# Performance work log

Hardware: AMD Instinct MI355X
Metric: run time of the kernel (lower is better)

Reference implementation:

```python
import jax, jax.numpy as jnp
import numpy as np

N, E, IN_DIM, HID, HEADS = 50000, 800000, 128, 16, 8
EPS_BN = 1e-5


def _gat_conv(x, edge_index, W, att_src, att_dst, bias, heads, out_ch, concat):
    # x: [N, F_in]; W: [heads*out_ch, F_in]; att_*: [heads, out_ch]
    n = x.shape[0]
    h = (x @ W.T).reshape(n, heads, out_ch)            # [N, H, C]
    a_src = (h * att_src[None]).sum(-1)                # [N, H]
    a_dst = (h * att_dst[None]).sum(-1)                # [N, H]
    src, dst = edge_index[0], edge_index[1]
    alpha = jax.nn.leaky_relu(a_src[src] + a_dst[dst], negative_slope=0.2)  # [E, H]
    # segment softmax over destination node (per head)
    amax = jax.ops.segment_max(alpha, dst, num_segments=n)
    amax = jnp.where(jnp.isfinite(amax), amax, 0.0)
    ex = jnp.exp(alpha - amax[dst])
    denom = jax.ops.segment_sum(ex, dst, num_segments=n)
    attn = ex / (denom[dst] + 1e-16)                   # [E, H]
    msg = h[src] * attn[:, :, None]                    # [E, H, C]
    out = jax.ops.segment_sum(msg, dst, num_segments=n)  # [N, H, C]
    out = out.reshape(n, heads * out_ch) if concat else out.mean(axis=1)
    return out + bias


def _bn_eval(h, mean, var, gamma, beta):
    return (h - mean) * jax.lax.rsqrt(var + EPS_BN) * gamma + beta


def setup_inputs() -> dict:
    key = jax.random.key(0)
    ks = jax.random.split(key, 16)
    s = 0.1
    inp = {
        "x": jax.random.normal(ks[0], (N, IN_DIM), jnp.float32),
        "edge_index": jax.random.randint(ks[1], (2, E), 0, N, jnp.int32),
        # layer 0: GATConv(128 -> 16, heads=8, concat)
        "w0": jax.random.normal(ks[2], (HEADS * HID, IN_DIM), jnp.float32) * s,
        "asrc0": jax.random.normal(ks[3], (HEADS, HID), jnp.float32) * s,
        "adst0": jax.random.normal(ks[4], (HEADS, HID), jnp.float32) * s,
        "b0": jnp.zeros((HEADS * HID,), jnp.float32),
        "skip0": jax.random.normal(ks[5], (HEADS * HID, IN_DIM), jnp.float32) * s,
        "bn0_g": jnp.ones((HEADS * HID,), jnp.float32),
        "bn0_b": jnp.zeros((HEADS * HID,), jnp.float32),
        "bn0_m": jax.random.normal(ks[6], (HEADS * HID,), jnp.float32) * s,
        "bn0_v": jax.random.uniform(ks[7], (HEADS * HID,), jnp.float32, 0.5, 1.5),
        # layer 1: GATConv(128 -> 16, heads=1, concat=False)
        "w1": jax.random.normal(ks[8], (HID, HEADS * HID), jnp.float32) * s,
        "asrc1": jax.random.normal(ks[9], (1, HID), jnp.float32) * s,
        "adst1": jax.random.normal(ks[10], (1, HID), jnp.float32) * s,
        "b1": jnp.zeros((HID,), jnp.float32),
        "skip1": jax.random.normal(ks[11], (HID, HEADS * HID), jnp.float32) * s,
        "bn1_g": jnp.ones((HID,), jnp.float32),
        "bn1_b": jnp.zeros((HID,), jnp.float32),
        "bn1_m": jax.random.normal(ks[12], (HID,), jnp.float32) * s,
        "bn1_v": jax.random.uniform(ks[13], (HID,), jnp.float32, 0.5, 1.5),
    }
    return inp


def reference(x, edge_index, w0, asrc0, adst0, b0, skip0, bn0_g, bn0_b, bn0_m, bn0_v,
              w1, asrc1, adst1, b1, skip1, bn1_g, bn1_b, bn1_m, bn1_v):
    # eval mode: dropout = identity, BN uses running stats
    h_in = x
    h = _gat_conv(h_in, edge_index, w0, asrc0, adst0, b0, HEADS, HID, True)   # [N, 128]
    h = _bn_eval(h, bn0_m, bn0_v, bn0_g, bn0_b)
    h = h + h_in @ skip0.T
    h = jax.nn.elu(h)
    h_in = h
    h = _gat_conv(h_in, edge_index, w1, asrc1, adst1, b1, 1, HID, False)      # [N, 16]
    h = _bn_eval(h, bn1_m, bn1_v, bn1_g, bn1_b)
    h = h + h_in @ skip1.T
    h = jax.nn.elu(h)
    return h
```

## Files before the change

### kernel.cpp

```cpp
#include <hip/hip_runtime.h>
#include <hip/hip_bf16.h>

#define NN 50000
#define EE 800000
#define INDIM 128
#define HIDC 16
#define NHEAD 8
#define COARSE 196
#define EPB 2048
#define CAPR 6144
#define CAPB 8192
#define CVT_BLKS 37

typedef __attribute__((ext_vector_type(8))) short bf16x8;
typedef __attribute__((ext_vector_type(4))) float f32x4;

__device__ __forceinline__ float bf2f(unsigned short u) {
    union { float f; unsigned int i; } v; v.i = ((unsigned int)u) << 16; return v.f;
}
__device__ __forceinline__ unsigned short f2bf(float f) {
    union { float f; unsigned int i; } v; v.f = f;
    unsigned int r = v.i + 0x7FFFu + ((v.i >> 16) & 1u);
    return (unsigned short)(r >> 16);
}

__global__ __launch_bounds__(256) void k_prep(
    const float* __restrict__ w0, const float* __restrict__ skip0,
    const float* __restrict__ w1, const float* __restrict__ skip1,
    const float* __restrict__ b0, const float* __restrict__ g0,
    const float* __restrict__ bb0, const float* __restrict__ m0,
    const float* __restrict__ v0,
    const float* __restrict__ b1, const float* __restrict__ g1,
    const float* __restrict__ bb1, const float* __restrict__ m1,
    const float* __restrict__ v1,
    unsigned int* __restrict__ wb2, unsigned int* __restrict__ wb1_2,
    float2* __restrict__ acb0, float2* __restrict__ acb1,
    const int* __restrict__ ei, int* __restrict__ ccur0,
    unsigned int* __restrict__ pairs)
{
    if (blockIdx.x < CVT_BLKS) {
        const long NW = 256 * 128 / 4;
        const long NW1 = 32 * 128 / 4;
        long i = (long)blockIdx.x * 256 + threadIdx.x;
        if (i < NW) {
            const float4* src = (i < 128 * 128 / 4) ? ((const float4*)w0 + i)
                                                    : ((const float4*)skip0 + (i - 128 * 128 / 4));
            float4 v = *src;
            wb2[i * 2]     = (unsigned int)f2bf(v.x) | ((unsigned int)f2bf(v.y) << 16);
            wb2[i * 2 + 1] = (unsigned int)f2bf(v.z) | ((unsigned int)f2bf(v.w) << 16);
        } else if (i < NW + NW1) {
            long j = i - NW;
            const float4* src = (j < 16 * 128 / 4) ? ((const float4*)w1 + j)
                                                   : ((const float4*)skip1 + (j - 16 * 128 / 4));
            float4 v = *src;
            wb1_2[j * 2]     = (unsigned int)f2bf(v.x) | ((unsigned int)f2bf(v.y) << 16);
            wb1_2[j * 2 + 1] = (unsigned int)f2bf(v.z) | ((unsigned int)f2bf(v.w) << 16);
        } else if (i < NW + NW1 + 128) {
            int c = (int)(i - NW - NW1);
            float A = g0[c] * rsqrtf(v0[c] + 1e-5f);
            acb0[c] = make_float2(A, (b0[c] - m0[c]) * A + bb0[c]);
        } else if (i < NW + NW1 + 128 + 16) {
            int c = (int)(i - NW - NW1 - 128);
            float A = g1[c] * rsqrtf(v1[c] + 1e-5f);
            acb1[c] = make_float2(A, (b1[c] - m1[c]) * A + bb1[c]);
        }
        return;
    }

    __shared__ int bcnt[256];
    __shared__ int lofs[256];
    __shared__ int gofs[256];
    __shared__ unsigned int stage[EPB];
    __shared__ int gpos[EPB];
    const int t = threadIdx.x;
    const int e0 = (blockIdx.x - CVT_BLKS) * EPB;

    bcnt[t] = 0;
    __syncthreads();

    int mybin[8], myrank[8];
    unsigned int mypair[8];
    #pragma unroll
    for (int k = 0; k < 8; k++) {
        int e = e0 + k * 256 + t;
        mybin[k] = -1;
        if (e < EE) {
            int s = ei[e], d = ei[EE + e];
            int b = d >> 8;
            myrank[k] = atomicAdd(&bcnt[b], 1);
            mybin[k] = b;
            mypair[k] = ((unsigned)d << 16) | (unsigned)s;
        }
    }
    __syncthreads();

    int v = bcnt[t];
    lofs[t] = v;
    __syncthreads();
    for (int off = 1; off < 256; off <<= 1) {
        int u = (t >= off) ? lofs[t - off] : 0;
        __syncthreads();
        lofs[t] += u;
        __syncthreads();
    }
    if (t < COARSE && v > 0)
        gofs[t] = t * CAPR + atomicAdd(&ccur0[t], v);
    __syncthreads();

    #pragma unroll
    for (int k = 0; k < 8; k++) {
        int b = mybin[k];
        if (b >= 0) {
            int slot = (lofs[b] - bcnt[b]) + myrank[k];
            stage[slot] = mypair[k];
            gpos[slot]  = gofs[b] + myrank[k];
        }
    }
    __syncthreads();

    const int total = lofs[255];
    for (int i = t; i < total; i += 256)
        pairs[gpos[i]] = stage[i];
}

__global__ __launch_bounds__(256) void k_mid(
    const unsigned int* __restrict__ pairs, const int* __restrict__ ccur0,
    unsigned short* __restrict__ srcidx, int* __restrict__ rowbeg,
    int* __restrict__ deg,
    const float* __restrict__ x, const unsigned short* __restrict__ wb,
    const float* __restrict__ asrc0, const float* __restrict__ adst0,
    unsigned char* __restrict__ h0f, unsigned short* __restrict__ s0b,
    float* __restrict__ a_src0, float* __restrict__ a_dst0)
{
    __shared__ int fcnt[256], fofs[256], fcur[256];
    __shared__ unsigned short stage[CAPB];

    if (blockIdx.x < COARSE) {
        const int b = blockIdx.x, t = threadIdx.x;
        const int beg = b * CAPR;
        int cnt = ccur0[b];
        if (cnt > CAPR) cnt = CAPR;

        fcnt[t] = 0;
        __syncthreads();
        for (int i = t; i < cnt; i += 256) {
            unsigned int d = pairs[beg + i] >> 16;
            atomicAdd(&fcnt[d & 255], 1);
        }
        __syncthreads();

        int v = fcnt[t];
        fofs[t] = v;
        __syncthreads();
        for (int off = 1; off < 256; off <<= 1) {
            int u = (t >= off) ? fofs[t - off] : 0;
            __syncthreads();
            fofs[t] += u;
            __syncthreads();
        }
        int ex = fofs[t] - v;
        int node = b * 256 + t;
        if (node < NN) { rowbeg[node] = beg + ex; deg[node] = v; }
        fcur[t] = ex;
        __syncthreads();

        for (int i = t; i < cnt; i += 256) {
            unsigned int p = pairs[beg + i];
            unsigned int d = p >> 16;
            int slot = atomicAdd(&fcur[d & 255], 1);
            stage[slot] = (unsigned short)(p & 0xFFFFu);
        }
        __syncthreads();
        for (int i = t; i < cnt; i += 256)
            srcidx[beg + i] = stage[i];
        return;
    }

    const int bid = blockIdx.x - COARSE;
    const int wave = threadIdx.x >> 6;
    const int lane = threadIdx.x & 63;
    const int lrow = lane & 15;
    const int quad = lane >> 4;
    const int rowbase = bid * 32;

    bf16x8 afrag[2][4];
    #pragma unroll
    for (int sub = 0; sub < 2; sub++) {
        const int row = min(rowbase + sub * 16 + lrow, NN - 1);
        const float* xr = x + (long)row * 128;
        #pragma unroll
        for (int ki = 0; ki < 4; ki++) {
            float4 a = *(const float4*)(xr + ki * 32 + quad * 8);
            float4 b = *(const float4*)(xr + ki * 32 + quad * 8 + 4);
            bf16x8 f;
            f[0] = (short)f2bf(a.x); f[1] = (short)f2bf(a.y);
            f[2] = (short)f2bf(a.z); f[3] = (short)f2bf(a.w);
            f[4] = (short)f2bf(b.x); f[5] = (short)f2bf(b.y);
            f[6] = (short)f2bf(b.z); f[7] = (short)f2bf(b.w);
            afrag[sub][ki] = f;
        }
    }

    #pragma unroll
    for (int t = 0; t < 4; t++) {
        const int jg = wave * 64 + t * 16 + lrow;
        bf16x8 bfrag[4];
        #pragma unroll
        for (int ki = 0; ki < 4; ki++)
            bfrag[ki] = *(const bf16x8*)(wb + (long)jg * 128 + ki * 32 + quad * 8);
        float4 asv = {0.f, 0.f, 0.f, 0.f}, adv = {0.f, 0.f, 0.f, 0.f};
        if (wave < 2) {
            const int cb = wave * 64 + t * 16 + quad * 4;
            asv = *(const float4*)(asrc0 + cb);
            adv = *(const float4*)(adst0 + cb);
        }
        #pragma unroll
        for (int sub = 0; sub < 2; sub++) {
            f32x4 acc = (f32x4){0.f, 0.f, 0.f, 0.f};
            #pragma unroll
            for (int ki = 0; ki < 4; ki++)
                acc = __builtin_amdgcn_mfma_f32_16x16x32_bf16(bfrag[ki], afrag[sub][ki], acc, 0, 0, 0);

            const int node = rowbase + sub * 16 + lrow;
            if (node < NN) {
                if (wave < 2) {
                    const int cb = wave * 64 + t * 16 + quad * 4;
                    unsigned int u = __builtin_amdgcn_cvt_pk_fp8_f32(acc[0], acc[1], 0u, 0);
                    u = __builtin_amdgcn_cvt_pk_fp8_f32(acc[2], acc[3], u, 1);
                    *(unsigned int*)(h0f + (long)node * 128 + cb) = u;
                    float ps = acc[0] * asv.x + acc[1] * asv.y + acc[2] * asv.z + acc[3] * asv.w;
                    float pd = acc[0] * adv.x + acc[1] * adv.y + acc[2] * adv.z + acc[3] * adv.w;
                    ps += __shfl_xor(ps, 16); ps += __shfl_xor(ps, 32);
                    pd += __shfl_xor(pd, 16); pd += __shfl_xor(pd, 32);
                    if (quad == 0) {
                        const int h = wave * 4 + t;
                        a_src0[(long)node * 8 + h] = ps;
                        a_dst0[(long)node * 8 + h] = pd;
                    }
                } else {
                    const int cb = (wave - 2) * 64 + t * 16 + quad * 4;
                    uint2 u;
                    u.x = (unsigned int)f2bf(acc[0]) | ((unsigned int)f2bf(acc[1]) << 16);
                    u.y = (unsigned int)f2bf(acc[2]) | ((unsigned int)f2bf(acc[3]) << 16);
                    *(uint2*)(s0b + (long)node * 128 + cb) = u;
                }
            }
        }
    }
}

__global__ __launch_bounds__(256) void k_agg0(
    const int* __restrict__ rowbeg, const int* __restrict__ deg,
    const unsigned short* __restrict__ srcidx,
    const unsigned char* __restrict__ h0f, const float* __restrict__ a_src0,
    const float* __restrict__ a_dst0, const unsigned short* __restrict__ s0b,
    const float2* __restrict__ acb0, unsigned int* __restrict__ hab2)
{
    const int d = (blockIdx.x * 256 + threadIdx.x) >> 6;
    if (d >= NN) return;
    const int lane = threadIdx.x & 63;
    const int beg = rowbeg[d], end = beg + deg[d];
    const int eslot = lane >> 3;
    const int hph1 = lane & 7;
    const int c = lane * 2;
    const int hsel = lane >> 3;
    const float adst = a_dst0[(long)d * 8 + hph1];

    float den = 0.f;
    float2 accA = {0.f, 0.f}, accB = {0.f, 0.f};
    for (int i = beg; i < end; i += 16) {
        const int idxA = i + eslot;
        const int idxB = i + 8 + eslot;
        const bool vA = idxA < end;
        const bool vB = idxB < end;
        const int sA = vA ? (int)srcidx[idxA] : 0;
        const int sB = vB ? (int)srcidx[idxB] : 0;
        float aA = a_src0[(long)sA * 8 + hph1] + adst;
        float aB = a_src0[(long)sB * 8 + hph1] + adst;
        aA = aA > 0.f ? aA : 0.2f * aA;
        aB = aB > 0.f ? aB : 0.2f * aB;
        const float wA = vA ? __expf(aA) : 0.f;
        const float wB = vB ? __expf(aB) : 0.f;
        den += wA + wB;
        #pragma unroll
        for (int j = 0; j < 8; j++) {
            const float wjA = __shfl(wA, j * 8 + hsel);
            const int sjA = __shfl(sA, j * 8);
            const float wjB = __shfl(wB, j * 8 + hsel);
            const int sjB = __shfl(sB, j * 8);
            const unsigned int uA = *(const unsigned short*)(h0f + (long)sjA * 128 + c);
            const unsigned int uB = *(const unsigned short*)(h0f + (long)sjB * 128 + c);
            accA.x += wjA * __builtin_amdgcn_cvt_f32_fp8(uA, 0);
            accA.y += wjA * __builtin_amdgcn_cvt_f32_fp8(uA, 1);
            accB.x += wjB * __builtin_amdgcn_cvt_f32_fp8(uB, 0);
            accB.y += wjB * __builtin_amdgcn_cvt_f32_fp8(uB, 1);
        }
    }
    float2 acc = {accA.x + accB.x, accA.y + accB.y};
    den += __shfl_xor(den, 8);
    den += __shfl_xor(den, 16);
    den += __shfl_xor(den, 32);
    const float denh = __shfl(den, hsel);
    const float inv = 1.f / (denh + 1e-16f);

    const float4 ab = *(const float4*)((const float*)acb0 + 2 * c);
    const unsigned int s0u = *(const unsigned int*)(s0b + (long)d * 128 + c);
    float x0 = acc.x * inv * ab.x + ab.y + bf2f((unsigned short)s0u);
    float x1 = acc.y * inv * ab.z + ab.w + bf2f((unsigned short)(s0u >> 16));
    x0 = x0 > 0.f ? x0 : __expf(x0) - 1.f;
    x1 = x1 > 0.f ? x1 : __expf(x1) - 1.f;
    hab2[(long)d * 64 + lane] =
        (unsigned int)f2bf(x0) | ((unsigned int)f2bf(x1) << 16);
}

__global__ __launch_bounds__(256) void k_post0(
    const unsigned short* __restrict__ hab,
    const unsigned short* __restrict__ wb1,
    const float* __restrict__ asrc1, const float* __restrict__ adst1,
    unsigned short* __restrict__ h1b, float* __restrict__ s1,
    float* __restrict__ a_src1, float* __restrict__ a_dst1)
{
    const int tid = threadIdx.x;
    const int lane = tid & 63, wave = tid >> 6;
    const int lrow = lane & 15, quad = lane >> 4;

    bf16x8 bfrag[2][4];
    #pragma unroll
    for (int t = 0; t < 2; t++)
        #pragma unroll
        for (int ki = 0; ki < 4; ki++)
            bfrag[t][ki] = *(const bf16x8*)(wb1 + (long)(t * 16 + lrow) * 128 + ki * 32 + quad * 8);
    const float avec = asrc1[lrow];
    const float dvec = adst1[lrow];

    const int tile = blockIdx.x * 4 + wave;
    if (tile * 16 >= NN) return;
    const int n0 = tile * 16;
    const long arow = (long)(n0 + lrow) * 128;

    bf16x8 afrag[4];
    #pragma unroll
    for (int ki = 0; ki < 4; ki++)
        afrag[ki] = *(const bf16x8*)(hab + arow + ki * 32 + quad * 8);

    f32x4 acc0 = (f32x4){0.f, 0.f, 0.f, 0.f};
    f32x4 acc1 = (f32x4){0.f, 0.f, 0.f, 0.f};
    #pragma unroll
    for (int ki = 0; ki < 4; ki++) {
        acc0 = __builtin_amdgcn_mfma_f32_16x16x32_bf16(afrag[ki], bfrag[0][ki], acc0, 0, 0, 0);
        acc1 = __builtin_amdgcn_mfma_f32_16x16x32_bf16(afrag[ki], bfrag[1][ki], acc1, 0, 0, 0);
    }

    #pragma unroll
    for (int r = 0; r < 4; r++) {
        const int node = n0 + quad * 4 + r;
        h1b[(long)node * 16 + lrow] = f2bf(acc0[r]);
        s1[(long)node * 16 + lrow] = acc1[r];
        float ps = acc0[r] * avec;
        float pd = acc0[r] * dvec;
        ps += __shfl_xor(ps, 1); ps += __shfl_xor(ps, 2);
        ps += __shfl_xor(ps, 4); ps += __shfl_xor(ps, 8);
        pd += __shfl_xor(pd, 1); pd += __shfl_xor(pd, 2);
        pd += __shfl_xor(pd, 4); pd += __shfl_xor(pd, 8);
        if (lrow == 0) { a_src1[node] = ps; a_dst1[node] = pd; }
    }
}

__global__ __launch_bounds__(256) void k_agg1_final(
    const int* __restrict__ rowbeg, const int* __restrict__ deg,
    const unsigned short* __restrict__ srcidx,
    const unsigned short* __restrict__ h1b, const float* __restrict__ a_src1,
    const float* __restrict__ a_dst1, const float* __restrict__ s1,
    const float2* __restrict__ acb1, float* __restrict__ out)
{
    const int gid = blockIdx.x * 256 + threadIdx.x;
    const int d = gid >> 3;
    if (d >= NN) return;
    const int lane = threadIdx.x & 63;
    const int gl = lane & 7;
    const int gb = lane & ~7;
    const int c0 = gl * 2;
    const int beg = rowbeg[d], end = beg + deg[d];
    const float adst = a_dst1[d];

    float den = 0.f;
    float2 accA = {0.f, 0.f}, accB = {0.f, 0.f};
    for (int i = beg; i < end; i += 16) {
        const int idxA = i + gl;
        const int idxB = i + 8 + gl;
        const bool vA = idxA < end;
        const bool vB = idxB < end;
        const int sA = vA ? (int)srcidx[idxA] : 0;
        const int sB = vB ? (int)srcidx[idxB] : 0;
        float aA = a_src1[sA] + adst;
        float aB = a_src1[sB] + adst;
        aA = aA > 0.f ? aA : 0.2f * aA;
        aB = aB > 0.f ? aB : 0.2f * aB;
        const float wA = vA ? __expf(aA) : 0.f;
        const float wB = vB ? __expf(aB) : 0.f;
        den += wA + wB;
        #pragma unroll
        for (int j = 0; j < 8; j++) {
            const float wjA = __shfl(wA, gb | j);
            const int sjA = __shfl(sA, gb | j);
            const float wjB = __shfl(wB, gb | j);
            const int sjB = __shfl(sB, gb | j);
            const unsigned int uA = *(const unsigned int*)(h1b + (long)sjA * 16 + c0);
            const unsigned int uB = *(const unsigned int*)(h1b + (long)sjB * 16 + c0);
            accA.x += wjA * bf2f((unsigned short)uA);
            accA.y += wjA * bf2f((unsigned short)(uA >> 16));
            accB.x += wjB * bf2f((unsigned short)uB);
            accB.y += wjB * bf2f((unsigned short)(uB >> 16));
        }
    }
    float2 acc = {accA.x + accB.x, accA.y + accB.y};
    den += __shfl_xor(den, 1);
    den += __shfl_xor(den, 2);
    den += __shfl_xor(den, 4);
    const float inv = 1.f / (den + 1e-16f);

    const float4 ab = *(const float4*)((const float*)acb1 + 2 * c0);
    float2 sv = *(const float2*)(s1 + (long)d * 16 + c0);
    float v0o = acc.x * inv * ab.x + ab.y + sv.x;
    float v1o = acc.y * inv * ab.z + ab.w + sv.y;
    v0o = v0o > 0.f ? v0o : __expf(v0o) - 1.f;
    v1o = v1o > 0.f ? v1o : __expf(v1o) - 1.f;
    *(float2*)(out + (long)d * 16 + c0) = make_float2(v0o, v1o);
}

extern "C" void kernel_launch(void* const* d_in, const int* in_sizes, int n_in,
                              void* d_out, int out_size, void* d_ws, size_t ws_size,
                              hipStream_t stream)
{
    (void)in_sizes; (void)n_in; (void)out_size; (void)ws_size;
    const float* x     = (const float*)d_in[0];
    const int*   ei    = (const int*)d_in[1];
    const float* w0    = (const float*)d_in[2];
    const float* asrc0 = (const float*)d_in[3];
    const float* adst0 = (const float*)d_in[4];
    const float* b0    = (const float*)d_in[5];
    const float* skip0 = (const float*)d_in[6];
    const float* bn0g  = (const float*)d_in[7];
    const float* bn0b  = (const float*)d_in[8];
    const float* bn0m  = (const float*)d_in[9];
    const float* bn0v  = (const float*)d_in[10];
    const float* w1    = (const float*)d_in[11];
    const float* asrc1 = (const float*)d_in[12];
    const float* adst1 = (const float*)d_in[13];
    const float* b1    = (const float*)d_in[14];
    const float* skip1 = (const float*)d_in[15];
    const float* bn1g  = (const float*)d_in[16];
    const float* bn1b  = (const float*)d_in[17];
    const float* bn1m  = (const float*)d_in[18];
    const float* bn1v  = (const float*)d_in[19];

    const long NPAIR = (long)COARSE * CAPR;
    unsigned int* pairs = (unsigned int*)d_ws;
    unsigned short* wb    = (unsigned short*)(pairs + NPAIR);
    unsigned short* wb1   = wb + 256 * 128;
    unsigned short* s0b   = wb1 + 32 * 128;
    unsigned short* hab   = s0b + (long)NN * 128;
    unsigned short* h1b   = hab + (long)NN * 128;
    unsigned short* srcidx= h1b + (long)NN * 16;
    unsigned char*  h0f   = (unsigned char*)(srcidx + NPAIR);
    float* a_src0 = (float*)(h0f + (long)NN * 128);
    float* a_dst0 = a_src0 + (long)NN * 8;
    float* s1     = a_dst0 + (long)NN * 8;
    float* a_src1 = s1 + (long)NN * 16;
    float* a_dst1 = a_src1 + NN;
    float2* acb0  = (float2*)(a_dst1 + NN);
    float2* acb1  = acb0 + 128;
    int* ccur0  = (int*)(acb1 + 16);
    int* rowbeg = ccur0 + COARSE;
    int* deg    = rowbeg + NN;

    hipMemsetAsync(ccur0, 0, (size_t)COARSE * 4, stream);

    const int PREP_BLKS = CVT_BLKS + (EE + EPB - 1) / EPB;
    k_prep<<<PREP_BLKS, 256, 0, stream>>>(
        w0, skip0, w1, skip1,
        b0, bn0g, bn0b, bn0m, bn0v, b1, bn1g, bn1b, bn1m, bn1v,
        (unsigned int*)wb, (unsigned int*)wb1, acb0, acb1,
        ei, ccur0, pairs);

    const int MID_BLKS = COARSE + (NN + 31) / 32;
    k_mid<<<MID_BLKS, 256, 0, stream>>>(
        pairs, ccur0, srcidx, rowbeg, deg,
        x, wb, asrc0, adst0, h0f, s0b, a_src0, a_dst0);

    k_agg0<<<(NN * 64 + 255) / 256, 256, 0, stream>>>(rowbeg, deg, srcidx, h0f,
                                                      a_src0, a_dst0, s0b, acb0,
                                                      (unsigned int*)hab);
    k_post0<<<(NN / 16 + 3) / 4, 256, 0, stream>>>(hab, wb1, asrc1, adst1,
                                                   h1b, s1, a_src1, a_dst1);
    k_agg1_final<<<(NN * 8 + 255) / 256, 256, 0, stream>>>(rowbeg, deg, srcidx, h1b,
                                                           a_src1, a_dst1, s1,
                                                           acb1, (float*)d_out);
}
```

Baseline: 204.9 us.

## Fuse layer-0 aggregation with layer-1 projection via shared-memory tile

Merges the layer-0 attention aggregation kernel and the layer-1 MFMA projection kernel into one kernel. Each block aggregates 16 destination nodes (4 per wave), stages the bf16 ELU outputs in padded LDS, then two waves run the MFMA for the layer-1 weights and skip projection. This removes the global round trip of the N×128 bf16 intermediate and one kernel launch. In exchange, each wave handles four nodes in sequence, which lowers parallelism per node and adds a block barrier where the two MFMA waves wait on the slowest aggregation wave.

```diff
diff --git a/kernel.cpp b/kernel.cpp
--- a/kernel.cpp
+++ b/kernel.cpp
@@ -11,6 +11,7 @@
 #define CAPR 6144
 #define CAPB 8192
 #define CVT_BLKS 37
+#define HSTRIDE 136
 
 typedef __attribute__((ext_vector_type(8))) short bf16x8;
 typedef __attribute__((ext_vector_type(4))) float f32x4;
@@ -249,120 +250,123 @@
     }
 }
 
-__global__ __launch_bounds__(256) void k_agg0(
+__global__ __launch_bounds__(256) void k_layer0(
     const int* __restrict__ rowbeg, const int* __restrict__ deg,
     const unsigned short* __restrict__ srcidx,
     const unsigned char* __restrict__ h0f, const float* __restrict__ a_src0,
     const float* __restrict__ a_dst0, const unsigned short* __restrict__ s0b,
-    const float2* __restrict__ acb0, unsigned int* __restrict__ hab2)
-{
-    const int d = (blockIdx.x * 256 + threadIdx.x) >> 6;
-    if (d >= NN) return;
-    const int lane = threadIdx.x & 63;
-    const int beg = rowbeg[d], end = beg + deg[d];
-    const int eslot = lane >> 3;
-    const int hph1 = lane & 7;
-    const int c = lane * 2;
-    const int hsel = lane >> 3;
-    const float adst = a_dst0[(long)d * 8 + hph1];
-
-    float den = 0.f;
-    float2 accA = {0.f, 0.f}, accB = {0.f, 0.f};
-    for (int i = beg; i < end; i += 16) {
-        const int idxA = i + eslot;
-        const int idxB = i + 8 + eslot;
-        const bool vA = idxA < end;
-        const bool vB = idxB < end;
-        const int sA = vA ? (int)srcidx[idxA] : 0;
-        const int sB = vB ? (int)srcidx[idxB] : 0;
-        float aA = a_src0[(long)sA * 8 + hph1] + adst;
-        float aB = a_src0[(long)sB * 8 + hph1] + adst;
-        aA = aA > 0.f ? aA : 0.2f * aA;
-        aB = aB > 0.f ? aB : 0.2f * aB;
-        const float wA = vA ? __expf(aA) : 0.f;
-        const float wB = vB ? __expf(aB) : 0.f;
-        den += wA + wB;
-        #pragma unroll
-        for (int j = 0; j < 8; j++) {
-            const float wjA = __shfl(wA, j * 8 + hsel);
-            const int sjA = __shfl(sA, j * 8);
-            const float wjB = __shfl(wB, j * 8 + hsel);
-            const int sjB = __shfl(sB, j * 8);
-            const unsigned int uA = *(const unsigned short*)(h0f + (long)sjA * 128 + c);
-            const unsigned int uB = *(const unsigned short*)(h0f + (long)sjB * 128 + c);
-            accA.x += wjA * __builtin_amdgcn_cvt_f32_fp8(uA, 0);
-            accA.y += wjA * __builtin_amdgcn_cvt_f32_fp8(uA, 1);
-            accB.x += wjB * __builtin_amdgcn_cvt_f32_fp8(uB, 0);
-            accB.y += wjB * __builtin_amdgcn_cvt_f32_fp8(uB, 1);
-        }
-    }
-    float2 acc = {accA.x + accB.x, accA.y + accB.y};
-    den += __shfl_xor(den, 8);
-    den += __shfl_xor(den, 16);
-    den += __shfl_xor(den, 32);
-    const float denh = __shfl(den, hsel);
-    const float inv = 1.f / (denh + 1e-16f);
-
-    const float4 ab = *(const float4*)((const float*)acb0 + 2 * c);
-    const unsigned int s0u = *(const unsigned int*)(s0b + (long)d * 128 + c);
-    float x0 = acc.x * inv * ab.x + ab.y + bf2f((unsigned short)s0u);
-    float x1 = acc.y * inv * ab.z + ab.w + bf2f((unsigned short)(s0u >> 16));
-    x0 = x0 > 0.f ? x0 : __expf(x0) - 1.f;
-    x1 = x1 > 0.f ? x1 : __expf(x1) - 1.f;
-    hab2[(long)d * 64 + lane] =
-        (unsigned int)f2bf(x0) | ((unsigned int)f2bf(x1) << 16);
-}
-
-__global__ __launch_bounds__(256) void k_post0(
-    const unsigned short* __restrict__ hab,
+    const float2* __restrict__ acb0,
     const unsigned short* __restrict__ wb1,
     const float* __restrict__ asrc1, const float* __restrict__ adst1,
     unsigned short* __restrict__ h1b, float* __restrict__ s1,
     float* __restrict__ a_src1, float* __restrict__ a_dst1)
 {
+    __shared__ unsigned short hls[16 * HSTRIDE];
     const int tid = threadIdx.x;
     const int lane = tid & 63, wave = tid >> 6;
     const int lrow = lane & 15, quad = lane >> 4;
-
-    bf16x8 bfrag[2][4];
+    const int n0 = blockIdx.x * 16;
+
+    bf16x8 bfrag[4];
+    float avec = 0.f, dvec = 0.f;
+    if (wave < 2) {
+        #pragma unroll
+        for (int ki = 0; ki < 4; ki++)
+            bfrag[ki] = *(const bf16x8*)(wb1 + (long)(wave * 16 + lrow) * 128 + ki * 32 + quad * 8);
+        avec = asrc1[lrow];
+        dvec = adst1[lrow];
+    }
+
+    const int eslot = lane >> 3;
+    const int hph1 = lane & 7;
+    const int c = lane * 2;
+    const int hsel = lane >> 3;
+    const float4 ab = *(const float4*)((const float*)acb0 + 2 * c);
+
     #pragma unroll
-    for (int t = 0; t < 2; t++)
+    for (int k = 0; k < 4; k++) {
+        const int d = n0 + wave * 4 + k;
+        const int beg = rowbeg[d], end = beg + deg[d];
+        const float adst = a_dst0[(long)d * 8 + hph1];
+
+        float den = 0.f;
+        float2 accA = {0.f, 0.f}, accB = {0.f, 0.f};
+        for (int i = beg; i < end; i += 16) {
+            const int idxA = i + eslot;
+            const int idxB = i + 8 + eslot;
+            const bool vA = idxA < end;
+            const bool vB = idxB < end;
+            const int sA = vA ? (int)srcidx[idxA] : 0;
+            const int sB = vB ? (int)srcidx[idxB] : 0;
+            float aA = a_src0[(long)sA * 8 + hph1] + adst;
+            float aB = a_src0[(long)sB * 8 + hph1] + adst;
+            aA = aA > 0.f ? aA : 0.2f * aA;
+            aB = aB > 0.f ? aB : 0.2f * aB;
+            const float wA = vA ? __expf(aA) : 0.f;
+            const float wB = vB ? __expf(aB) : 0.f;
+            den += wA + wB;
+            #pragma unroll
+            for (int j = 0; j < 8; j++) {
+                const float wjA = __shfl(wA, j * 8 + hsel);
+                const int sjA = __shfl(sA, j * 8);
+                const float wjB = __shfl(wB, j * 8 + hsel);
+                const int sjB = __shfl(sB, j * 8);
+                const unsigned int uA = *(const unsigned short*)(h0f + (long)sjA * 128 + c);
+                const unsigned int uB = *(const unsigned short*)(h0f + (long)sjB * 128 + c);
+                accA.x += wjA * __builtin_amdgcn_cvt_f32_fp8(uA, 0);
+                accA.y += wjA * __builtin_amdgcn_cvt_f32_fp8(uA, 1);
+                accB.x += wjB * __builtin_amdgcn_cvt_f32_fp8(uB, 0);
+                accB.y += wjB * __builtin_amdgcn_cvt_f32_fp8(uB, 1);
+            }
+        }
+        float2 acc = {accA.x + accB.x, accA.y + accB.y};
+        den += __shfl_xor(den, 8);
+        den += __shfl_xor(den, 16);
+        den += __shfl_xor(den, 32);
+        const float denh = __shfl(den, hsel);
+        const float inv = 1.f / (denh + 1e-16f);
+
+        const unsigned int s0u = *(const unsigned int*)(s0b + (long)d * 128 + c);
+        float x0 = acc.x * inv * ab.x + ab.y + bf2f((unsigned short)s0u);
+        float x1 = acc.y * inv * ab.z + ab.w + bf2f((unsigned short)(s0u >> 16));
+        x0 = x0 > 0.f ? x0 : __expf(x0) - 1.f;
+        x1 = x1 > 0.f ? x1 : __expf(x1) - 1.f;
+        *(unsigned int*)&hls[(wave * 4 + k) * HSTRIDE + c] =
+            (unsigned int)f2bf(x0) | ((unsigned int)f2bf(x1) << 16);
+    }
+    __syncthreads();
+
+    if (wave < 2) {
+        bf16x8 afrag[4];
         #pragma unroll
         for (int ki = 0; ki < 4; ki++)
-            bfrag[t][ki] = *(const bf16x8*)(wb1 + (long)(t * 16 + lrow) * 128 + ki * 32 + quad * 8);
-    const float avec = asrc1[lrow];
-    const float dvec = adst1[lrow];
-
-    const int tile = blockIdx.x * 4 + wave;
-    if (tile * 16 >= NN) return;
-    const int n0 = tile * 16;
-    const long arow = (long)(n0 + lrow) * 128;
-
-    bf16x8 afrag[4];
-    #pragma unroll
-    for (int ki = 0; ki < 4; ki++)
-        afrag[ki] = *(const bf16x8*)(hab + arow + ki * 32 + quad * 8);
-
-    f32x4 acc0 = (f32x4){0.f, 0.f, 0.f, 0.f};
-    f32x4 acc1 = (f32x4){0.f, 0.f, 0.f, 0.f};
-    #pragma unroll
-    for (int ki = 0; ki < 4; ki++) {
-        acc0 = __builtin_amdgcn_mfma_f32_16x16x32_bf16(afrag[ki], bfrag[0][ki], acc0, 0, 0, 0);
-        acc1 = __builtin_amdgcn_mfma_f32_16x16x32_bf16(afrag[ki], bfrag[1][ki], acc1, 0, 0, 0);
-    }
-
-    #pragma unroll
-    for (int r = 0; r < 4; r++) {
-        const int node = n0 + quad * 4 + r;
-        h1b[(long)node * 16 + lrow] = f2bf(acc0[r]);
-        s1[(long)node * 16 + lrow] = acc1[r];
-        float ps = acc0[r] * avec;
-        float pd = acc0[r] * dvec;
-        ps += __shfl_xor(ps, 1); ps += __shfl_xor(ps, 2);
-        ps += __shfl_xor(ps, 4); ps += __shfl_xor(ps, 8);
-        pd += __shfl_xor(pd, 1); pd += __shfl_xor(pd, 2);
-        pd += __shfl_xor(pd, 4); pd += __shfl_xor(pd, 8);
-        if (lrow == 0) { a_src1[node] = ps; a_dst1[node] = pd; }
+            afrag[ki] = *(const bf16x8*)&hls[lrow * HSTRIDE + ki * 32 + quad * 8];
+
+        f32x4 acc = (f32x4){0.f, 0.f, 0.f, 0.f};
+        #pragma unroll
+        for (int ki = 0; ki < 4; ki++)
+            acc = __builtin_amdgcn_mfma_f32_16x16x32_bf16(afrag[ki], bfrag[ki], acc, 0, 0, 0);
+
+        if (wave == 0) {
+            #pragma unroll
+            for (int r = 0; r < 4; r++) {
+                const int node = n0 + quad * 4 + r;
+                h1b[(long)node * 16 + lrow] = f2bf(acc[r]);
+                float ps = acc[r] * avec;
+                float pd = acc[r] * dvec;
+                ps += __shfl_xor(ps, 1); ps += __shfl_xor(ps, 2);
+                ps += __shfl_xor(ps, 4); ps += __shfl_xor(ps, 8);
+                pd += __shfl_xor(pd, 1); pd += __shfl_xor(pd, 2);
+                pd += __shfl_xor(pd, 4); pd += __shfl_xor(pd, 8);
+                if (lrow == 0) { a_src1[node] = ps; a_dst1[node] = pd; }
+            }
+        } else {
+            #pragma unroll
+            for (int r = 0; r < 4; r++) {
+                const int node = n0 + quad * 4 + r;
+                s1[(long)node * 16 + lrow] = acc[r];
+            }
+        }
     }
 }
 
@@ -459,8 +463,7 @@
     unsigned short* wb    = (unsigned short*)(pairs + NPAIR);
     unsigned short* wb1   = wb + 256 * 128;
     unsigned short* s0b   = wb1 + 32 * 128;
-    unsigned short* hab   = s0b + (long)NN * 128;
-    unsigned short* h1b   = hab + (long)NN * 128;
+    unsigned short* h1b   = s0b + (long)NN * 128;
     unsigned short* srcidx= h1b + (long)NN * 16;
     unsigned char*  h0f   = (unsigned char*)(srcidx + NPAIR);
     float* a_src0 = (float*)(h0f + (long)NN * 128);
@@ -488,11 +491,11 @@
         pairs, ccur0, srcidx, rowbeg, deg,
         x, wb, asrc0, adst0, h0f, s0b, a_src0, a_dst0);
 
-    k_agg0<<<(NN * 64 + 255) / 256, 256, 0, stream>>>(rowbeg, deg, srcidx, h0f,
-                                                      a_src0, a_dst0, s0b, acb0,
-                                                      (unsigned int*)hab);
-    k_post0<<<(NN / 16 + 3) / 4, 256, 0, stream>>>(hab, wb1, asrc1, adst1,
-                                                   h1b, s1, a_src1, a_dst1);
+    k_layer0<<<NN / 16, 256, 0, stream>>>(rowbeg, deg, srcidx, h0f,
+                                          a_src0, a_dst0, s0b, acb0,
+                                          wb1, asrc1, adst1,
+                                          h1b, s1, a_src1, a_dst1);
+
     k_agg1_final<<<(NN * 8 + 255) / 256, 256, 0, stream>>>(rowbeg, deg, srcidx, h1b,
                                                            a_src1, a_dst1, s1,
                                                            acb1, (float*)d_out);
```

After: 224.8 us. +9.7%, slower.
